# Performance work log

Measured on AMD Instinct MI355X. Metric: run time of the kernel, lower is better.

## Reference

```python
import jax, jax.numpy as jnp
import numpy as np

GRID = 128
N0 = 262144
CHANNELS = [16, 32, 64, 128, 256]
EPS = 1e-5
OFFS2 = [(dx, dy, dz) for dx in (0, 1) for dy in (0, 1) for dz in (0, 1)]
OFFS3 = [(dx, dy, dz) for dx in (-1, 0, 1) for dy in (-1, 0, 1) for dz in (-1, 0, 1)]


def _keys(c, size):
    return (c[:, 0].astype(np.int64) * size + c[:, 1]) * size + c[:, 2]


def _rulebook(in_coords, out_coords, offsets, size_in, stride):
    # explicit-GEMM rulebook: for each kernel offset, (input_idx, output_idx) pairs,
    # padded to n_out with a validity mask so shapes are static.
    ik = _keys(in_coords, size_in)
    order = np.argsort(ik)
    sk = ik[order]
    K, P = len(offsets), out_coords.shape[0]
    I = np.zeros((K, P), np.int32)
    O = np.zeros((K, P), np.int32)
    M = np.zeros((K, P), bool)
    for k, off in enumerate(offsets):
        nbr = out_coords * stride + np.asarray(off)
        valid = np.all((nbr >= 0) & (nbr < size_in), axis=1)
        nk = _keys(np.clip(nbr, 0, size_in - 1), size_in)
        pos = np.minimum(np.searchsorted(sk, nk), len(sk) - 1)
        found = valid & (sk[pos] == nk)
        cnt = int(found.sum())
        I[k, :cnt] = order[pos[found]]
        O[k, :cnt] = np.nonzero(found)[0]
        M[k, :cnt] = True
    return I, O, M


def setup_inputs() -> dict:
    rng = np.random.RandomState(0)
    flat = rng.choice(GRID ** 3, size=N0, replace=False)
    coords = np.stack([flat // (GRID * GRID), (flat // GRID) % GRID, flat % GRID], 1).astype(np.int64)
    key = jax.random.key(0)
    ctr = [0]
    def nrm(shape, scale=1.0):
        ctr[0] += 1
        return scale * jax.random.normal(jax.random.fold_in(key, ctr[0]), shape, jnp.float32)
    inp = {"x": nrm((N0, CHANNELS[0]))}
    size = GRID
    for l in range(4):
        cin, cout = CHANNELS[l], CHANNELS[l + 1]
        out_coords = np.unique(coords // 2, axis=0)
        dI, dO, dM = _rulebook(coords, out_coords, OFFS2, size, 2)       # stride-2, k=2 down conv
        bI, bO, bM = _rulebook(out_coords, out_coords, OFFS3, size // 2, 1)  # stride-1, k=3 block conv
        inp[f"dW{l}"] = nrm((8, cin, cout), (8 * cin) ** -0.5)
        inp[f"dI{l}"] = jnp.asarray(dI); inp[f"dO{l}"] = jnp.asarray(dO); inp[f"dM{l}"] = jnp.asarray(dM)
        inp[f"dG{l}"] = 1.0 + nrm((cout,), 0.1)
        inp[f"dB{l}"] = nrm((cout,), 0.1)
        inp[f"dN{l}"] = int(out_coords.shape[0])
        inp[f"bW{l}"] = nrm((27, cout, cout), (27 * cout) ** -0.5)
        inp[f"bC{l}"] = nrm((cout,), 0.01)
        inp[f"bI{l}"] = jnp.asarray(bI); inp[f"bO{l}"] = jnp.asarray(bO); inp[f"bM{l}"] = jnp.asarray(bM)
        inp[f"bG{l}"] = 1.0 + nrm((cout,), 0.1)
        inp[f"bH{l}"] = nrm((cout,), 0.1)
        coords = out_coords
        size //= 2
    return inp


def _conv(f, W, I, O, M, n_out, bias=None):
    # gather -> GEMM -> scatter-add, one pass per kernel offset (fixed small K)
    out = jnp.zeros((n_out, W.shape[-1]), f.dtype)
    for k in range(W.shape[0]):
        g = jnp.where(M[k][:, None], f[I[k]], 0.0)
        out = out.at[O[k]].add(g @ W[k])
    return out if bias is None else out + bias


def _bn_relu(f, g, b):
    # training-mode BatchNorm over active voxels, fused with ReLU
    m = f.mean(0)
    v = jnp.mean((f - m) ** 2, 0)
    return jax.nn.relu((f - m) * (g * jax.lax.rsqrt(v + EPS)) + b)


def _forward(x, levels):
    outs = [x]
    for (dW, dI, dO, dM, dG, dB, dN, bW, bC, bI, bO, bM, bG, bH) in levels:
        x = _bn_relu(_conv(x, dW, dI, dO, dM, dN), dG, dB)        # down block (bias=False)
        x = _bn_relu(_conv(x, bW, bI, bO, bM, dN, bC), bG, bH)    # ConvBlock
        outs.append(x)
    return tuple(outs)


def reference(x, dW0, dI0, dO0, dM0, dG0, dB0, dN0, bW0, bC0, bI0, bO0, bM0, bG0, bH0,
              dW1, dI1, dO1, dM1, dG1, dB1, dN1, bW1, bC1, bI1, bO1, bM1, bG1, bH1,
              dW2, dI2, dO2, dM2, dG2, dB2, dN2, bW2, bC2, bI2, bO2, bM2, bG2, bH2,
              dW3, dI3, dO3, dM3, dG3, dB3, dN3, bW3, bC3, bI3, bO3, bM3, bG3, bH3):
    levels = [
        (dW0, dI0, dO0, dM0, dG0, dB0, dN0, bW0, bC0, bI0, bO0, bM0, bG0, bH0),
        (dW1, dI1, dO1, dM1, dG1, dB1, dN1, bW1, bC1, bI1, bO1, bM1, bG1, bH1),
        (dW2, dI2, dO2, dM2, dG2, dB2, dN2, bW2, bC2, bI2, bO2, bM2, bG2, bH2),
        (dW3, dI3, dO3, dM3, dG3, dB3, dN3, bW3, bC3, bI3, bO3, bM3, bG3, bH3),
    ]
    return _forward(x, levels)
```

## Files before the change

### kernel.cpp

```cpp
#include <hip/hip_runtime.h>
#include <hip/hip_bf16.h>
#include <stdint.h>
#include <stddef.h>

typedef __hip_bfloat16 bf16;
typedef __attribute__((ext_vector_type(8))) short bf8_t;
typedef __attribute__((ext_vector_type(4))) float f4_t;
static const int CH[5] = {16, 32, 64, 128, 256};

__device__ __forceinline__ float b2f(unsigned short u) {
    return __uint_as_float(((unsigned int)u) << 16);
}
__device__ __forceinline__ unsigned short f2bu(float f) {
    union { bf16 h; unsigned short u; } cv;
    cv.h = __float2bfloat16(f);
    return cv.u;
}
__device__ __forceinline__ void fma4(float4& a, float s, const float4& w) {
    a.x = fmaf(s, w.x, a.x);
    a.y = fmaf(s, w.y, a.y);
    a.z = fmaf(s, w.z, a.z);
    a.w = fmaf(s, w.w, a.w);
}
struct us4 { unsigned short a, b, c, d; };

__global__ void k_sentinel(float* __restrict__ out, float v) {
    if (threadIdx.x == 0) out[0] = v;
}

__global__ void SparseConvEncoder_20633022890309_kernel(
        const unsigned char* __restrict__ bM0, int* __restrict__ flag) {
    if (threadIdx.x == 0) {
        flag[0] = 1;
        flag[1] = 0;
        flag[2] = (bM0[0] == 1 && bM0[1] == 0 && bM0[2] == 0 && bM0[3] == 0 && bM0[4] == 1) ? 1 : 0;
    }
}

__global__ void __launch_bounds__(256) k_copy(const float* __restrict__ x,
                                              float* __restrict__ y, long n) {
    long i = (long)blockIdx.x * 256 + threadIdx.x;
    if (i < n) y[i] = x[i];
}

__global__ void __launch_bounds__(256) k_copytob(const float* __restrict__ x,
                                                 float* __restrict__ y,
                                                 unsigned short* __restrict__ yb, long n) {
    long i = (long)blockIdx.x * 256 + threadIdx.x;
    if (i < n) {
        float v = x[i];
        y[i] = v;
        yb[i] = f2bu(v);
    }
}

__global__ void __launch_bounds__(256) k_wt2(const float* __restrict__ dW,
                                             unsigned short* __restrict__ dWt, int dcin,
                                             const float* __restrict__ bW,
                                             unsigned short* __restrict__ bWt, int bcin,
                                             int cout, long dtot, long btot) {
    long i = (long)blockIdx.x * 256 + threadIdx.x;
    if (i < dtot) {
        long cc = (long)dcin * cout;
        int k = (int)(i / cc);
        int rem = (int)(i % cc);
        int co = rem / dcin, ci = rem % dcin;
        dWt[i] = f2bu(dW[((long)k * dcin + ci) * cout + co]);
    } else if (i < dtot + btot) {
        long j = i - dtot;
        long cc = (long)bcin * cout;
        int k = (int)(j / cc);
        int rem = (int)(j % cc);
        int co = rem / bcin, ci = rem % bcin;
        bWt[j] = f2bu(bW[((long)k * bcin + ci) * cout + co]);
    }
}

__global__ void __launch_bounds__(256) k_scatter(const int* __restrict__ I,
                                                 const int* __restrict__ O,
                                                 const void* __restrict__ M,
                                                 const int* __restrict__ flag,
                                                 int* __restrict__ R, int P, int k0, int cnt) {
    int i = blockIdx.x * 256 + threadIdx.x;
    if (i >= cnt) return;
    long gi = (long)k0 * P + i;
    int m = flag[2] ? ((const int*)M)[gi] : (int)((const unsigned char*)M)[gi];
    if (!m) return;
    R[(long)(i / P) * P + O[gi]] = I[gi];
}

__global__ void __launch_bounds__(256) k_init(float* __restrict__ out,
                                              const float* __restrict__ bias,
                                              long total, int maskC) {
    long i = (long)blockIdx.x * 256 + threadIdx.x;
    if (i < total) out[i] = bias ? bias[i & maskC] : 0.f;
}

template <int CIN, int TN, int MODE, int KT>
__global__ void __launch_bounds__(256, 2) k_mconv(const unsigned short* __restrict__ Xb,
                                                  const unsigned short* __restrict__ Wt,
                                                  const float* __restrict__ bias,
                                                  const int* __restrict__ R,
                                                  float* __restrict__ out,
                                                  int n, int cout, int kcnt, int gs) {
    const int lane = threadIdx.x & 63;
    const int wave = threadIdx.x >> 6;
    const int rt = blockIdx.x * 4 + wave;
    const int row_tiles = (n + 15) >> 4;
    if (rt >= row_tiles) return;
    const int m = lane & 15, q = lane >> 4;
    const int o = rt * 16 + m;
    const int co0 = blockIdx.y * (16 * TN);
    const bf8_t zero = {};

    f4_t acc[TN];
#pragma unroll
    for (int t = 0; t < TN; ++t) {
        if (MODE == 0) {
            float bv = bias ? bias[co0 + t * 16 + m] : 0.f;
            acc[t][0] = bv; acc[t][1] = bv; acc[t][2] = bv; acc[t][3] = bv;
        } else if (MODE == 1) {
#pragma unroll
            for (int g = 0; g < 4; ++g) {
                int row = rt * 16 + q * 4 + g;
                acc[t][g] = (row < n) ? out[(long)row * cout + co0 + t * 16 + m] : 0.f;
            }
        } else {
            acc[t][0] = 0.f; acc[t][1] = 0.f; acc[t][2] = 0.f; acc[t][3] = 0.f;
        }
    }

    bool touched = (MODE != 2);

    if constexpr (KT > 0) {
        int r[KT];
#pragma unroll
        for (int kk = 0; kk < KT; ++kk)
            r[kk] = (o < n) ? R[(long)kk * n + o] : -1;

        if constexpr (CIN == 16) {
            bf8_t a[KT / 2];
#pragma unroll
            for (int p = 0; p < KT / 2; ++p) {
                int rsel = (q < 2) ? r[2 * p] : r[2 * p + 1];
                long ax = (long)((rsel >= 0) ? rsel : 0) * CIN + (q & 1) * 8;
                bf8_t av = *(const bf8_t*)(Xb + ax);
                a[p] = (rsel >= 0) ? av : zero;
            }
            __builtin_amdgcn_sched_barrier(0);
#pragma unroll
            for (int p = 0; p < KT / 2; ++p) {
                int ksel = 2 * p + (q >> 1);
#pragma unroll
                for (int t = 0; t < TN; ++t) {
                    int co = co0 + t * 16 + m;
                    long bx = ((long)ksel * cout + co) * CIN + (q & 1) * 8;
                    bf8_t b = *(const bf8_t*)(Wt + bx);
                    acc[t] = __builtin_amdgcn_mfma_f32_16x16x32_bf16(a[p], b, acc[t], 0, 0, 0);
                }
            }
        } else {
            constexpr int NC = CIN / 32;
            constexpr int GB = (KT * NC * 4 <= 128) ? KT : 9;
            constexpr int NG = (KT + GB - 1) / GB;

#define PRE_GRP(A, G0)                                                              \
    _Pragma("unroll")                                                               \
    for (int j = 0; j < GB; ++j) {                                                  \
        _Pragma("unroll")                                                           \
        for (int cb = 0; cb < NC; ++cb) {                                           \
            int kk = (G0) + j;                                                      \
            long ax = (long)((r[kk] >= 0) ? r[kk] : 0) * CIN + cb * 32 + q * 8;     \
            bf8_t av = *(const bf8_t*)(Xb + ax);                                    \
            A[j][cb] = (r[kk] >= 0) ? av : zero;                                    \
        }                                                                           \
    }

#define CMP_GRP(A, G0)                                                              \
    _Pragma("unroll")                                                               \
    for (int j = 0; j < GB; ++j) {                                                  \
        _Pragma("unroll")                                                           \
        for (int cb = 0; cb < NC; ++cb) {                                           \
            _Pragma("unroll")                                                       \
            for (int t = 0; t < TN; ++t) {                                          \
                int kk = (G0) + j;                                                  \
                int co = co0 + t * 16 + m;                                          \
                long bx = ((long)kk * cout + co) * CIN + cb * 32 + q * 8;           \
                bf8_t b = *(const bf8_t*)(Wt + bx);                                 \
                acc[t] = __builtin_amdgcn_mfma_f32_16x16x32_bf16(A[j][cb], b,       \
                                                                 acc[t], 0, 0, 0);  \
            }                                                                       \
        }                                                                           \
    }

            if constexpr (NG == 1) {
                bf8_t a0[GB][NC];
                PRE_GRP(a0, 0)
                __builtin_amdgcn_sched_barrier(0);
                CMP_GRP(a0, 0)
            } else {
                static_assert(NG == 3, "phase structure assumes 3 groups");
                bf8_t a0[GB][NC];
                bf8_t a1[GB][NC];
                bf8_t a2[GB][NC];
                PRE_GRP(a0, 0)
                PRE_GRP(a1, GB)
                __builtin_amdgcn_sched_barrier(0);
                CMP_GRP(a0, 0)
                __builtin_amdgcn_sched_barrier(0);
                PRE_GRP(a2, 2 * GB)
                __builtin_amdgcn_sched_barrier(0);
                CMP_GRP(a1, GB)
                __builtin_amdgcn_sched_barrier(0);
                CMP_GRP(a2, 2 * GB)
            }
#undef PRE_GRP
#undef CMP_GRP
        }
    } else {
        int ks = 0, ke = kcnt;
        if (MODE == 2) {
            ks = blockIdx.z * gs;
            ke = ks + gs;
            if (ke > kcnt) ke = kcnt;
        }
        constexpr int NC = (CIN >= 32) ? (CIN / 32) : 1;
        constexpr int JB = (CIN >= 128) ? 2 : 4;
        for (int kb = ks; kb < ke; kb += JB) {
            int rj[JB];
#pragma unroll
            for (int j = 0; j < JB; ++j) {
                int kk = kb + j;
                rj[j] = (kk < ke && o < n) ? R[(long)kk * n + o] : -1;
            }
            if (MODE == 2) {
                int any = 0;
#pragma unroll
                for (int j = 0; j < JB; ++j) any |= (rj[j] >= 0) ? 1 : 0;
                if (__ballot(any) == 0ULL) continue;
                touched = true;
            }
            bf8_t a[JB][NC];
#pragma unroll
            for (int j = 0; j < JB; ++j) {
                int kk = kb + j;
                bool inb = (kk < ke) && (rj[j] >= 0);
#pragma unroll
                for (int cb = 0; cb < NC; ++cb) {
                    const bool kval = !(CIN == 16 && q >= 2);
                    const int kbase = (CIN == 16) ? (kval ? q * 8 : 0) : (cb * 32 + q * 8);
                    long ax = (long)(inb ? rj[j] : 0) * CIN + kbase;
                    bf8_t av = *(const bf8_t*)(Xb + ax);
                    a[j][cb] = (inb && kval) ? av : zero;
                }
            }
            __builtin_amdgcn_sched_barrier(0);
#pragma unroll
            for (int j = 0; j < JB; ++j) {
                int kk = kb + j;
                if (kk >= ke) break;
#pragma unroll
                for (int cb = 0; cb < NC; ++cb) {
                    const bool kval = !(CIN == 16 && q >= 2);
                    const int kbase = (CIN == 16) ? (kval ? q * 8 : 0) : (cb * 32 + q * 8);
#pragma unroll
                    for (int t = 0; t < TN; ++t) {
                        int co = co0 + t * 16 + m;
                        long bx = ((long)kk * cout + co) * CIN + kbase;
                        bf8_t bv = *(const bf8_t*)(Wt + bx);
                        bf8_t b = kval ? bv : zero;
                        acc[t] = __builtin_amdgcn_mfma_f32_16x16x32_bf16(a[j][cb], b,
                                                                         acc[t], 0, 0, 0);
                    }
                }
            }
        }
    }

    if (MODE == 2 && !touched) return;
#pragma unroll
    for (int t = 0; t < TN; ++t) {
#pragma unroll
        for (int g = 0; g < 4; ++g) {
            int row = rt * 16 + q * 4 + g;
            if (row >= n) continue;
            float* p = out + (long)row * cout + co0 + t * 16 + m;
            if (MODE == 2) atomicAdd(p, acc[t][g]);
            else *p = acc[t][g];
        }
    }
}

static void mconv_dispatch(int cin, int tn, int mode, int kt, dim3 grd,
                           const unsigned short* Xb, const unsigned short* Wt,
                           const float* bias, const int* R, float* out,
                           int n, int cout, int kcnt, int gs, hipStream_t stream) {
#define MF_(CC, TT, KK)                                                            \
    if (cin == CC && tn == TT && mode == 0 && kt == KK) {                          \
        k_mconv<CC, TT, 0, KK><<<grd, 256, 0, stream>>>(Xb, Wt, bias, R, out, n,   \
                                                        cout, kcnt, gs);           \
        return;                                                                    \
    }
    MF_(16, 2, 8) MF_(32, 2, 8) MF_(32, 4, 8) MF_(64, 2, 8) MF_(64, 4, 8)
    MF_(32, 2, 27) MF_(64, 2, 27) MF_(64, 4, 27)
#undef MF_
#define M3_(CC, TT, MM)                                                            \
    if (cin == CC && tn == TT && mode == MM) {                                     \
        k_mconv<CC, TT, MM, 0><<<grd, 256, 0, stream>>>(Xb, Wt, bias, R, out, n,   \
                                                        cout, kcnt, gs);           \
        return;                                                                    \
    }
#define M2_(CC) M3_(CC, 2, 0) M3_(CC, 2, 1) M3_(CC, 2, 2) \
                M3_(CC, 4, 0) M3_(CC, 4, 1) M3_(CC, 4, 2)
    M2_(16) M2_(32) M2_(64) M2_(128) M2_(256)
#undef M2_
#undef M3_
}

static void run_mconv(const unsigned short* Xb, const unsigned short* Wt,
                      const float* bias, const int* I, const int* O, const void* M,
                      const int* flag, int* R, float* out, int n, int cin, int cout,
                      int K, int G, hipStream_t stream) {
    int rt = (n + 15) / 16;
    int bx = (rt + 3) / 4;
    int tn = (cout >= 64) ? 4 : 2;
    int gy = cout / (16 * tn);
    long bxy = (long)bx * gy;
    int kg = 1;
    if (bxy < 512 && G >= K) {
        kg = (int)((1024 + bxy - 1) / bxy);
        if (kg > K) kg = K;
    }
    int gs = (K + kg - 1) / kg;
    kg = (K + gs - 1) / gs;

    if (kg > 1) {
        int cnt = K * n;
        hipMemsetAsync(R, 0xFF, (size_t)cnt * 4, stream);
        k_scatter<<<(cnt + 255) / 256, 256, 0, stream>>>(I, O, M, flag, R, n, 0, cnt);
        long tot = (long)n * cout;
        k_init<<<(int)((tot + 255) / 256), 256, 0, stream>>>(out, bias, tot, cout - 1);
        mconv_dispatch(cin, tn, 2, 0, dim3(bx, gy, kg), Xb, Wt, bias, R, out,
                       n, cout, K, gs, stream);
    } else {
        for (int k0 = 0; k0 < K; k0 += G) {
            int g = (K - k0 < G) ? (K - k0) : G;
            int cnt = g * n;
            hipMemsetAsync(R, 0xFF, (size_t)cnt * 4, stream);
            k_scatter<<<(cnt + 255) / 256, 256, 0, stream>>>(I, O, M, flag, R, n, k0, cnt);
            int kt = (k0 == 0 && g == K) ? K : 0;
            mconv_dispatch(cin, tn, (k0 == 0) ? 0 : 1, kt, dim3(bx, gy, 1), Xb,
                           Wt + (size_t)k0 * cout * cin, bias, R, out,
                           n, cout, g, g, stream);
        }
    }
}

template <int CIN, int ROWS, int XBF, int MODE>
__global__ void __launch_bounds__(256) k_conv_t(const void* __restrict__ X,
                                                const float* __restrict__ W,
                                                const float* __restrict__ bias,
                                                const int* __restrict__ R,
                                                float* __restrict__ out,
                                                int n, int cout,
                                                int wk0, int kcnt, int gs) {
    const int c4 = threadIdx.x;
    const int by = blockDim.y;
    const int base = blockIdx.x * by * ROWS;
    const float* Xf = (const float*)X;
    const unsigned short* Xb = (const unsigned short*)X;

    int o[ROWS];
    float4 acc[ROWS];
    bool touched[ROWS];
#pragma unroll
    for (int j = 0; j < ROWS; ++j) {
        o[j] = base + j * by + threadIdx.y;
        touched[j] = false;
        acc[j] = make_float4(0.f, 0.f, 0.f, 0.f);
        if (o[j] < n) {
            if (MODE == 0) {
                if (bias) acc[j] = *(const float4*)(bias + c4 * 4);
            } else if (MODE == 1) {
                acc[j] = *(const float4*)(out + (long)o[j] * cout + c4 * 4);
            }
        }
    }
    int ks = 0, ke = kcnt;
    if (MODE == 2) {
        ks = blockIdx.y * gs;
        ke = ks + gs;
        if (ke > kcnt) ke = kcnt;
    }
    for (int kk = ks; kk < ke; ++kk) {
        int r[ROWS];
        bool any = false;
#pragma unroll
        for (int j = 0; j < ROWS; ++j) {
            r[j] = (o[j] < n) ? R[(long)kk * n + o[j]] : -1;
            any = any || (r[j] >= 0);
            touched[j] = touched[j] || (r[j] >= 0);
        }
        if (!any) continue;
        const float* wk = W + ((long)(wk0 + kk) * CIN) * cout + c4 * 4;
#pragma unroll
        for (int ci = 0; ci < CIN; ci += 4) {
            float4 w0 = *(const float4*)(wk + (long)(ci + 0) * cout);
            float4 w1 = *(const float4*)(wk + (long)(ci + 1) * cout);
            float4 w2 = *(const float4*)(wk + (long)(ci + 2) * cout);
            float4 w3 = *(const float4*)(wk + (long)(ci + 3) * cout);
#pragma unroll
            for (int j = 0; j < ROWS; ++j) {
                if (r[j] < 0) continue;
                float x0, x1, x2, x3;
                if (XBF) {
                    us4 u = *(const us4*)(Xb + (long)r[j] * CIN + ci);
                    x0 = b2f(u.a); x1 = b2f(u.b); x2 = b2f(u.c); x3 = b2f(u.d);
                } else {
                    float4 xv = *(const float4*)(Xf + (long)r[j] * CIN + ci);
                    x0 = xv.x; x1 = xv.y; x2 = xv.z; x3 = xv.w;
                }
                fma4(acc[j], x0, w0);
                fma4(acc[j], x1, w1);
                fma4(acc[j], x2, w2);
                fma4(acc[j], x3, w3);
            }
        }
    }
#pragma unroll
    for (int j = 0; j < ROWS; ++j) {
        if (o[j] >= n) continue;
        if (MODE == 2) {
            if (!touched[j]) continue;
            float* p = out + (long)o[j] * cout + c4 * 4;
            atomicAdd(p + 0, acc[j].x);
            atomicAdd(p + 1, acc[j].y);
            atomicAdd(p + 2, acc[j].z);
            atomicAdd(p + 3, acc[j].w);
        } else {
            *(float4*)(out + (long)o[j] * cout + c4 * 4) = acc[j];
        }
    }
}

static void conv_dispatch(int cin, int rows, int xbf, int mode, dim3 grd, dim3 blk,
                          const void* X, const float* W, const float* bias,
                          const int* R, float* out, int n, int cout,
                          int wk0, int kcnt, int gs, hipStream_t stream) {
#define C3_(CC, RR, XB, MM)                                                        \
    if (cin == CC && rows == RR && xbf == XB && mode == MM) {                      \
        k_conv_t<CC, RR, XB, MM><<<grd, blk, 0, stream>>>(X, W, bias, R, out, n,   \
                                                          cout, wk0, kcnt, gs);    \
        return;                                                                    \
    }
#define C2_(CC, RR) C3_(CC, RR, 0, 0) C3_(CC, RR, 0, 1) C3_(CC, RR, 0, 2) \
                    C3_(CC, RR, 1, 0) C3_(CC, RR, 1, 1) C3_(CC, RR, 1, 2)
#define C1_(CC) C2_(CC, 1) C2_(CC, 2) C2_(CC, 4)
    C1_(16) C1_(32) C1_(64) C1_(128) C1_(256)
#undef C1_
#undef C2_
#undef C3_
}

static void run_conv(const void* X, int xbf, const float* W, const float* bias,
                     const int* I, const int* O, const void* M, const int* flag,
                     int* R, float* out, int n, int cin, int cout, int K,
                     int G, hipStream_t stream) {
    int bx = cout / 4, by = 256 / bx;
    int g4 = (n + by * 4 - 1) / (by * 4);
    int g2 = (n + by * 2 - 1) / (by * 2);
    int rows;
    if (g4 >= 1024) rows = 4;
    else if (g2 >= 1024) rows = 2;
    else rows = 1;
    int gridn = (n + by * rows - 1) / (by * rows);
    int kg = 1;
    if (gridn < 768 && G >= K) {
        kg = (2048 + gridn - 1) / gridn;
        if (kg > K) kg = K;
    }
    int gs = (K + kg - 1) / kg;
    kg = (K + gs - 1) / gs;
    dim3 blk(bx, by);
    if (kg > 1) {
        int cnt = K * n;
        hipMemsetAsync(R, 0xFF, (size_t)cnt * 4, stream);
        k_scatter<<<(cnt + 255) / 256, 256, 0, stream>>>(I, O, M, flag, R, n, 0, cnt);
        long tot = (long)n * cout;
        k_init<<<(int)((tot + 255) / 256), 256, 0, stream>>>(out, bias, tot, cout - 1);
        conv_dispatch(cin, rows, xbf, 2, dim3(gridn, kg), blk, X, W, bias, R, out,
                      n, cout, 0, K, gs, stream);
    } else {
        for (int k0 = 0; k0 < K; k0 += G) {
            int g = (K - k0 < G) ? (K - k0) : G;
            int cnt = g * n;
            hipMemsetAsync(R, 0xFF, (size_t)cnt * 4, stream);
            k_scatter<<<(cnt + 255) / 256, 256, 0, stream>>>(I, O, M, flag, R, n, k0, cnt);
            conv_dispatch(cin, rows, xbf, (k0 == 0) ? 0 : 1, dim3(gridn, 1), blk,
                          X, W, bias, R, out, n, cout, k0, g, g, stream);
        }
    }
}

__global__ void __launch_bounds__(256) k_stats(const float* __restrict__ X,
                                               float* __restrict__ sums, int n, int C) {
    int c = threadIdx.x, ty = threadIdx.y, ny = blockDim.y;
    float s1 = 0.f, s2 = 0.f;
    for (int o = blockIdx.x * ny + ty; o < n; o += gridDim.x * ny) {
        float v = X[(long)o * C + c];
        s1 += v;
        s2 += v * v;
    }
    __shared__ float sm[512];
    sm[ty * C + c] = s1;
    sm[256 + ty * C + c] = s2;
    __syncthreads();
    if (ty == 0) {
        for (int t = 1; t < ny; ++t) {
            s1 += sm[t * C + c];
            s2 += sm[256 + t * C + c];
        }
        atomicAdd(&sums[c], s1);
        atomicAdd(&sums[C + c], s2);
    }
}

__global__ void __launch_bounds__(256) k_apply(const float* __restrict__ X,
                                               const float* __restrict__ sums,
                                               const float* __restrict__ g,
                                               const float* __restrict__ b,
                                               void* __restrict__ Y, int ybf,
                                               unsigned short* __restrict__ Y2,
                                               long total, int maskC, int C, float inv_n) {
    long i = (long)blockIdx.x * 256 + threadIdx.x;
    if (i >= total) return;
    int c = (int)(i & (long)maskC);
    float mean = sums[c] * inv_n;
    float var = fmaf(-mean, mean, sums[C + c] * inv_n);
    float sc = g[c] * rsqrtf(var + 1e-5f);
    float sh = fmaf(-mean, sc, b[c]);
    float v = fmaf(X[i], sc, sh);
    v = v > 0.f ? v : 0.f;
    if (ybf) ((unsigned short*)Y)[i] = f2bu(v);
    else     ((float*)Y)[i] = v;
    if (Y2) Y2[i] = f2bu(v);
}

static void run_bn(const float* src, int n, int C, const float* g, const float* b,
                   void* dst, int dst_bf16, unsigned short* dst2,
                   float* sums, hipStream_t stream) {
    hipMemsetAsync(sums, 0, 2 * C * sizeof(float), stream);
    dim3 sblk(C, 256 / C);
    int sgrd = (n + (int)sblk.y - 1) / (int)sblk.y;
    if (sgrd > 1024) sgrd = 1024;
    k_stats<<<sgrd, sblk, 0, stream>>>(src, sums, n, C);
    long tot = (long)n * C;
    k_apply<<<(int)((tot + 255) / 256), 256, 0, stream>>>(src, sums, g, b, dst, dst_bf16,
                                                          dst2, tot, C - 1, C,
                                                          1.0f / (float)n);
}

extern "C" void kernel_launch(void* const* d_in, const int* in_sizes, int n_in,
                              void* d_out, int out_size, void* d_ws, size_t ws_size,
                              hipStream_t stream) {
    float* out = (float*)d_out;

    int stride = 0;
    if (n_in == 57) stride = 14;
    else if (n_in == 53) stride = 13;
    if (!stride) {
        k_sentinel<<<1, 64, 0, stream>>>(out, 10240.f + (float)n_in);
        return;
    }
    static const int o14[13] = {0, 1, 2, 3, 4, 5, 7, 8, 9, 10, 11, 12, 13};
    static const int o13[13] = {0, 1, 2, 3, 4, 5, 6, 7, 8, 9, 10, 11, 12};
    const int* om = (stride == 14) ? o14 : o13;

    long n0 = (long)in_sizes[0];
    int P[4];
    bool ok = (n0 % 16 == 0);
    long total = n0;
    for (int l = 0; l < 4 && ok; ++l) {
        int base = 1 + stride * l;
        int sdI = in_sizes[base + om[1]], sdO = in_sizes[base + om[2]], sdM = in_sizes[base + om[3]];
        int sbI = in_sizes[base + om[8]], sbO = in_sizes[base + om[9]], sbM = in_sizes[base + om[10]];
        if (sdI <= 0 || sdI % 8 != 0 || sdO != sdI || sdM != sdI) { ok = false; break; }
        int p = sdI / 8;
        if (sbI != 27 * p || sbO != sbI || sbM != sbI) { ok = false; break; }
        if (in_sizes[base + om[0]] != 8 * CH[l] * CH[l + 1]) { ok = false; break; }
        if (in_sizes[base + om[6]] != 27 * CH[l + 1] * CH[l + 1]) { ok = false; break; }
        P[l] = p;
        total += (long)p * CH[l + 1];
    }
    if (!ok) {
        k_sentinel<<<1, 64, 0, stream>>>(out, 49152.f);
        return;
    }
    if (total != (long)out_size) {
        k_sentinel<<<1, 64, 0, stream>>>(out, 53248.f);
        return;
    }

    auto al = [](size_t x) { return (x + 255) / 256 * 256; };
    size_t maxBuf = 0, maxP = 0, maxXb = 0;
    long rowsIn[4] = {n0 / 16, P[0], P[1], P[2]};
    for (int l = 0; l < 4; ++l) {
        size_t b = (size_t)P[l] * CH[l + 1];
        if (b > maxBuf) maxBuf = b;
        if ((size_t)P[l] > maxP) maxP = (size_t)P[l];
        size_t xi = (size_t)rowsIn[l] * CH[l];
        if (xi > maxXb) maxXb = xi;
    }
    const size_t fixed = 4096;
    size_t rmin = al(maxP * 4);
    size_t dwt_sz = al((size_t)8 * 128 * 256 * 2);
    size_t bwt_sz = al((size_t)27 * 256 * 256 * 2);
    size_t mf_need = dwt_sz + bwt_sz + al(maxXb * 2) + al(maxBuf * 2) + fixed + rmin;

    if (ws_size >= mf_need) {
        char* wsp = (char*)d_ws;
        unsigned short* dWt = (unsigned short*)wsp; wsp += dwt_sz;
        unsigned short* bWt = (unsigned short*)wsp; wsp += bwt_sz;
        unsigned short* xb = (unsigned short*)wsp;  wsp += al(maxXb * 2);
        unsigned short* bufB = (unsigned short*)wsp; wsp += al(maxBuf * 2);
        float* sums = (float*)wsp; wsp += 1024;
        int* flag = (int*)wsp;     wsp += 2048;
        int* R = (int*)wsp;
        size_t Rbytes = ws_size - (size_t)(wsp - (char*)d_ws);

        SparseConvEncoder_20633022890309_kernel<<<1, 64, 0, stream>>>(
            (const unsigned char*)d_in[1 + om[10]], flag);
        k_copytob<<<(int)((n0 + 255) / 256), 256, 0, stream>>>((const float*)d_in[0],
                                                               out, xb, n0);

        long coff = n0;
        for (int l = 0; l < 4; ++l) {
            int base = 1 + stride * l;
            const float* dW = (const float*)d_in[base + om[0]];
            const int* dI = (const int*)d_in[base + om[1]];
            const int* dO = (const int*)d_in[base + om[2]];
            const void* dM = d_in[base + om[3]];
            const float* dG = (const float*)d_in[base + om[4]];
            const float* dB = (const float*)d_in[base + om[5]];
            const float* bW = (const float*)d_in[base + om[6]];
            const float* bC = (const float*)d_in[base + om[7]];
            const int* bI = (const int*)d_in[base + om[8]];
            const int* bO = (const int*)d_in[base + om[9]];
            const void* bM = d_in[base + om[10]];
            const float* bG = (const float*)d_in[base + om[11]];
            const float* bH = (const float*)d_in[base + om[12]];
            int n = P[l], cin = CH[l], cout = CH[l + 1];

            int G = (int)(Rbytes / ((size_t)n * 4));
            if (G > 27) G = 27;
            if (G < 1) G = 1;

            float* chunkp = out + coff;

            long dwtot = (long)8 * cin * cout;
            long bwtot = (long)27 * cout * cout;
            k_wt2<<<(int)((dwtot + bwtot + 255) / 256), 256, 0, stream>>>(
                dW, dWt, cin, bW, bWt, cout, cout, dwtot, bwtot);

            run_mconv(xb, dWt, nullptr, dI, dO, dM, flag, R, chunkp,
                      n, cin, cout, 8, (G > 8) ? 8 : G, stream);
            run_bn(chunkp, n, cout, dG, dB, bufB, 1, nullptr, sums, stream);

            run_mconv(bufB, bWt, bC, bI, bO, bM, flag, R, chunkp,
                      n, cout, cout, 27, G, stream);
            run_bn(chunkp, n, cout, bG, bH, chunkp, 0,
                   (l < 3) ? xb : nullptr, sums, stream);

            coff += (long)n * cout;
        }
        return;
    }

    int bufB_bf16;
    size_t bufBytes;
    if (ws_size >= fixed + al(maxBuf * 4) + rmin) { bufB_bf16 = 0; bufBytes = al(maxBuf * 4); }
    else if (ws_size >= fixed + al(maxBuf * 2) + rmin) { bufB_bf16 = 1; bufBytes = al(maxBuf * 2); }
    else {
        k_sentinel<<<1, 64, 0, stream>>>(out, 16384.f + (float)(ws_size >> 20));
        return;
    }
    size_t Rbytes = ws_size - fixed - bufBytes;
    char* wsp = (char*)d_ws;
    void* bufB = (void*)wsp;   wsp += bufBytes;
    float* sums = (float*)wsp; wsp += 1024;
    int* flag = (int*)wsp;     wsp += 2048;
    int* R = (int*)wsp;

    SparseConvEncoder_20633022890309_kernel<<<1, 64, 0, stream>>>(
        (const unsigned char*)d_in[1 + om[10]], flag);
    k_copy<<<(int)((n0 + 255) / 256), 256, 0, stream>>>((const float*)d_in[0], out, n0);

    long coff = n0;
    const void* cur_in = d_in[0];
    int cur_xbf = 0;
    for (int l = 0; l < 4; ++l) {
        int base = 1 + stride * l;
        const float* dW = (const float*)d_in[base + om[0]];
        const int* dI = (const int*)d_in[base + om[1]];
        const int* dO = (const int*)d_in[base + om[2]];
        const void* dM = d_in[base + om[3]];
        const float* dG = (const float*)d_in[base + om[4]];
        const float* dB = (const float*)d_in[base + om[5]];
        const float* bW = (const float*)d_in[base + om[6]];
        const float* bC = (const float*)d_in[base + om[7]];
        const int* bI = (const int*)d_in[base + om[8]];
        const int* bO = (const int*)d_in[base + om[9]];
        const void* bM = d_in[base + om[10]];
        const float* bG = (const float*)d_in[base + om[11]];
        const float* bH = (const float*)d_in[base + om[12]];
        int n = P[l], cin = CH[l], cout = CH[l + 1];

        int G = (int)(Rbytes / ((size_t)n * 4));
        if (G > 27) G = 27;
        if (G < 1) G = 1;

        float* chunkp = out + coff;
        run_conv(cur_in, cur_xbf, dW, nullptr, dI, dO, dM, flag, R, chunkp,
                 n, cin, cout, 8, (G > 8) ? 8 : G, stream);
        run_bn(chunkp, n, cout, dG, dB, bufB, bufB_bf16, nullptr, sums, stream);
        run_conv(bufB, bufB_bf16, bW, bC, bI, bO, bM, flag, R, chunkp,
                 n, cout, cout, 27, G, stream);
        run_bn(chunkp, n, cout, bG, bH, chunkp, 0, nullptr, sums, stream);

        cur_in = (const void*)chunkp;
        cur_xbf = 0;
        coff += (long)n * cout;
    }
}
```

Before: 822.1 us.

## Tile weights in MFMA fragment order and use a zero row for missing neighbors

Weights are reordered into per-lane MFMA fragment layout, so each wave's B loads become contiguous 512-byte reads instead of strided ones. The rulebook is padded to a multiple of 16 rows and filled with the index of an appended zero row instead of -1. This removes per-load validity selects and bounds checks in the gather loops. It also removes the early-skip ballot for empty kernel-offset chunks, so fully empty chunks now execute MFMAs, and it slightly loosens the split-K threshold.

```diff
diff --git a/kernel.cpp b/kernel.cpp
--- a/kernel.cpp
+++ b/kernel.cpp
@@ -54,6 +54,21 @@
     }
 }
 
+__device__ __forceinline__ long wt_tiled_src(long j, int cin, int cout) {
+    int e = (int)(j & 7);
+    int l = (int)((j >> 3) & 63);
+    int m = l & 15, q = l >> 4;
+    long u = j >> 9;
+    int NC = cin >> 5;
+    int cout16 = cout >> 4;
+    int cb = (int)(u % NC); u /= NC;
+    int ct = (int)(u % cout16);
+    int kk = (int)(u / cout16);
+    int ci = cb * 32 + q * 8 + e;
+    int co = ct * 16 + m;
+    return ((long)kk * cin + ci) * cout + co;
+}
+
 __global__ void __launch_bounds__(256) k_wt2(const float* __restrict__ dW,
                                              unsigned short* __restrict__ dWt, int dcin,
                                              const float* __restrict__ bW,
@@ -61,32 +76,40 @@
                                              int cout, long dtot, long btot) {
     long i = (long)blockIdx.x * 256 + threadIdx.x;
     if (i < dtot) {
-        long cc = (long)dcin * cout;
-        int k = (int)(i / cc);
-        int rem = (int)(i % cc);
-        int co = rem / dcin, ci = rem % dcin;
-        dWt[i] = f2bu(dW[((long)k * dcin + ci) * cout + co]);
+        if (dcin == 16) {
+            long cc = (long)dcin * cout;
+            int k = (int)(i / cc);
+            int rem = (int)(i % cc);
+            int co = rem / dcin, ci = rem % dcin;
+            dWt[i] = f2bu(dW[((long)k * dcin + ci) * cout + co]);
+        } else {
+            dWt[i] = f2bu(dW[wt_tiled_src(i, dcin, cout)]);
+        }
     } else if (i < dtot + btot) {
         long j = i - dtot;
-        long cc = (long)bcin * cout;
-        int k = (int)(j / cc);
-        int rem = (int)(j % cc);
-        int co = rem / bcin, ci = rem % bcin;
-        bWt[j] = f2bu(bW[((long)k * bcin + ci) * cout + co]);
-    }
+        bWt[j] = f2bu(bW[wt_tiled_src(j, bcin, cout)]);
+    }
+}
+
+__global__ void __launch_bounds__(256) k_prep(int* __restrict__ R, long cnt, int zr,
+                                              unsigned short* __restrict__ zrow, int zc) {
+    long i = (long)blockIdx.x * 256 + threadIdx.x;
+    if (i < cnt) R[i] = zr;
+    if (i < zc) zrow[i] = 0;
 }
 
 __global__ void __launch_bounds__(256) k_scatter(const int* __restrict__ I,
                                                  const int* __restrict__ O,
                                                  const void* __restrict__ M,
                                                  const int* __restrict__ flag,
-                                                 int* __restrict__ R, int P, int k0, int cnt) {
+                                                 int* __restrict__ R, int P, int S,
+                                                 int k0, int cnt) {
     int i = blockIdx.x * 256 + threadIdx.x;
     if (i >= cnt) return;
     long gi = (long)k0 * P + i;
     int m = flag[2] ? ((const int*)M)[gi] : (int)((const unsigned char*)M)[gi];
     if (!m) return;
-    R[(long)(i / P) * P + O[gi]] = I[gi];
+    R[(long)(i / P) * S + O[gi]] = I[gi];
 }
 
 __global__ void __launch_bounds__(256) k_init(float* __restrict__ out,
@@ -108,9 +131,12 @@
     const int rt = blockIdx.x * 4 + wave;
     const int row_tiles = (n + 15) >> 4;
     if (rt >= row_tiles) return;
+    const int n16 = row_tiles << 4;
     const int m = lane & 15, q = lane >> 4;
     const int o = rt * 16 + m;
     const int co0 = blockIdx.y * (16 * TN);
+    const int bt = blockIdx.y * TN;
+    const int cout16 = cout >> 4;
     const bf8_t zero = {};
 
     f4_t acc[TN];
@@ -130,22 +156,18 @@
         }
     }
 
-    bool touched = (MODE != 2);
-
     if constexpr (KT > 0) {
         int r[KT];
 #pragma unroll
         for (int kk = 0; kk < KT; ++kk)
-            r[kk] = (o < n) ? R[(long)kk * n + o] : -1;
+            r[kk] = R[(long)kk * n16 + o];
 
         if constexpr (CIN == 16) {
             bf8_t a[KT / 2];
 #pragma unroll
             for (int p = 0; p < KT / 2; ++p) {
                 int rsel = (q < 2) ? r[2 * p] : r[2 * p + 1];
-                long ax = (long)((rsel >= 0) ? rsel : 0) * CIN + (q & 1) * 8;
-                bf8_t av = *(const bf8_t*)(Xb + ax);
-                a[p] = (rsel >= 0) ? av : zero;
+                a[p] = *(const bf8_t*)(Xb + (long)rsel * CIN + (q & 1) * 8);
             }
             __builtin_amdgcn_sched_barrier(0);
 #pragma unroll
@@ -161,7 +183,7 @@
             }
         } else {
             constexpr int NC = CIN / 32;
-            constexpr int GB = (KT * NC * 4 <= 128) ? KT : 9;
+            constexpr int GB = (KT * NC * 4 <= 128) ? KT : ((KT > 9) ? 9 : KT);
             constexpr int NG = (KT + GB - 1) / GB;
 
 #define PRE_GRP(A, G0)                                                              \
@@ -169,10 +191,7 @@
     for (int j = 0; j < GB; ++j) {                                                  \
         _Pragma("unroll")                                                           \
         for (int cb = 0; cb < NC; ++cb) {                                           \
-            int kk = (G0) + j;                                                      \
-            long ax = (long)((r[kk] >= 0) ? r[kk] : 0) * CIN + cb * 32 + q * 8;     \
-            bf8_t av = *(const bf8_t*)(Xb + ax);                                    \
-            A[j][cb] = (r[kk] >= 0) ? av : zero;                                    \
+            A[j][cb] = *(const bf8_t*)(Xb + (long)r[(G0) + j] * CIN + cb * 32 + q * 8); \
         }                                                                           \
     }
 
@@ -183,9 +202,7 @@
         for (int cb = 0; cb < NC; ++cb) {                                           \
             _Pragma("unroll")                                                       \
             for (int t = 0; t < TN; ++t) {                                          \
-                int kk = (G0) + j;                                                  \
-                int co = co0 + t * 16 + m;                                          \
-                long bx = ((long)kk * cout + co) * CIN + cb * 32 + q * 8;           \
+                long bx = ((((long)((G0) + j) * cout16 + bt + t) * NC + cb) * 64 + lane) * 8; \
                 bf8_t b = *(const bf8_t*)(Wt + bx);                                 \
                 acc[t] = __builtin_amdgcn_mfma_f32_16x16x32_bf16(A[j][cb], b,       \
                                                                  acc[t], 0, 0, 0);  \
@@ -231,27 +248,20 @@
 #pragma unroll
             for (int j = 0; j < JB; ++j) {
                 int kk = kb + j;
-                rj[j] = (kk < ke && o < n) ? R[(long)kk * n + o] : -1;
-            }
-            if (MODE == 2) {
-                int any = 0;
-#pragma unroll
-                for (int j = 0; j < JB; ++j) any |= (rj[j] >= 0) ? 1 : 0;
-                if (__ballot(any) == 0ULL) continue;
-                touched = true;
+                int kc = (kk < ke) ? kk : (ke - 1);
+                rj[j] = R[(long)kc * n16 + o];
             }
             bf8_t a[JB][NC];
 #pragma unroll
             for (int j = 0; j < JB; ++j) {
-                int kk = kb + j;
-                bool inb = (kk < ke) && (rj[j] >= 0);
 #pragma unroll
                 for (int cb = 0; cb < NC; ++cb) {
-                    const bool kval = !(CIN == 16 && q >= 2);
-                    const int kbase = (CIN == 16) ? (kval ? q * 8 : 0) : (cb * 32 + q * 8);
-                    long ax = (long)(inb ? rj[j] : 0) * CIN + kbase;
-                    bf8_t av = *(const bf8_t*)(Xb + ax);
-                    a[j][cb] = (inb && kval) ? av : zero;
+                    if (CIN == 16) {
+                        a[j][cb] = (q < 2) ? *(const bf8_t*)(Xb + (long)rj[j] * CIN + q * 8)
+                                           : zero;
+                    } else {
+                        a[j][cb] = *(const bf8_t*)(Xb + (long)rj[j] * CIN + cb * 32 + q * 8);
+                    }
                 }
             }
             __builtin_amdgcn_sched_barrier(0);
@@ -261,14 +271,17 @@
                 if (kk >= ke) break;
 #pragma unroll
                 for (int cb = 0; cb < NC; ++cb) {
-                    const bool kval = !(CIN == 16 && q >= 2);
-                    const int kbase = (CIN == 16) ? (kval ? q * 8 : 0) : (cb * 32 + q * 8);
 #pragma unroll
                     for (int t = 0; t < TN; ++t) {
-                        int co = co0 + t * 16 + m;
-                        long bx = ((long)kk * cout + co) * CIN + kbase;
-                        bf8_t bv = *(const bf8_t*)(Wt + bx);
-                        bf8_t b = kval ? bv : zero;
+                        bf8_t b;
+                        if (CIN == 16) {
+                            int co = co0 + t * 16 + m;
+                            b = (q < 2) ? *(const bf8_t*)(Wt + ((long)kk * cout + co) * CIN + q * 8)
+                                        : zero;
+                        } else {
+                            long bx = ((((long)kk * cout16 + bt + t) * NC + cb) * 64 + lane) * 8;
+                            b = *(const bf8_t*)(Wt + bx);
+                        }
                         acc[t] = __builtin_amdgcn_mfma_f32_16x16x32_bf16(a[j][cb], b,
                                                                          acc[t], 0, 0, 0);
                     }
@@ -277,7 +290,6 @@
         }
     }
 
-    if (MODE == 2 && !touched) return;
 #pragma unroll
     for (int t = 0; t < TN; ++t) {
 #pragma unroll
@@ -317,27 +329,30 @@
 #undef M3_
 }
 
-static void run_mconv(const unsigned short* Xb, const unsigned short* Wt,
+static void run_mconv(unsigned short* Xb, int nin, const unsigned short* Wt,
                       const float* bias, const int* I, const int* O, const void* M,
                       const int* flag, int* R, float* out, int n, int cin, int cout,
                       int K, int G, hipStream_t stream) {
     int rt = (n + 15) / 16;
+    int n16 = rt * 16;
     int bx = (rt + 3) / 4;
     int tn = (cout >= 64) ? 4 : 2;
     int gy = cout / (16 * tn);
     long bxy = (long)bx * gy;
     int kg = 1;
-    if (bxy < 512 && G >= K) {
+    if (bxy <= 512 && G >= K) {
         kg = (int)((1024 + bxy - 1) / bxy);
         if (kg > K) kg = K;
     }
     int gs = (K + kg - 1) / kg;
     kg = (K + gs - 1) / gs;
+    unsigned short* zrow = Xb + (size_t)nin * cin;
 
     if (kg > 1) {
-        int cnt = K * n;
-        hipMemsetAsync(R, 0xFF, (size_t)cnt * 4, stream);
-        k_scatter<<<(cnt + 255) / 256, 256, 0, stream>>>(I, O, M, flag, R, n, 0, cnt);
+        long cnt = (long)K * n16;
+        k_prep<<<(int)((cnt + 255) / 256), 256, 0, stream>>>(R, cnt, nin, zrow, cin);
+        k_scatter<<<(K * n + 255) / 256, 256, 0, stream>>>(I, O, M, flag, R, n, n16,
+                                                           0, K * n);
         long tot = (long)n * cout;
         k_init<<<(int)((tot + 255) / 256), 256, 0, stream>>>(out, bias, tot, cout - 1);
         mconv_dispatch(cin, tn, 2, 0, dim3(bx, gy, kg), Xb, Wt, bias, R, out,
@@ -345,9 +360,10 @@
     } else {
         for (int k0 = 0; k0 < K; k0 += G) {
             int g = (K - k0 < G) ? (K - k0) : G;
-            int cnt = g * n;
-            hipMemsetAsync(R, 0xFF, (size_t)cnt * 4, stream);
-            k_scatter<<<(cnt + 255) / 256, 256, 0, stream>>>(I, O, M, flag, R, n, k0, cnt);
+            long cnt = (long)g * n16;
+            k_prep<<<(int)((cnt + 255) / 256), 256, 0, stream>>>(R, cnt, nin, zrow, cin);
+            k_scatter<<<(g * n + 255) / 256, 256, 0, stream>>>(I, O, M, flag, R, n, n16,
+                                                               k0, g * n);
             int kt = (k0 == 0 && g == K) ? K : 0;
             mconv_dispatch(cin, tn, (k0 == 0) ? 0 : 1, kt, dim3(bx, gy, 1), Xb,
                            Wt + (size_t)k0 * cout * cin, bias, R, out,
@@ -485,7 +501,7 @@
     if (kg > 1) {
         int cnt = K * n;
         hipMemsetAsync(R, 0xFF, (size_t)cnt * 4, stream);
-        k_scatter<<<(cnt + 255) / 256, 256, 0, stream>>>(I, O, M, flag, R, n, 0, cnt);
+        k_scatter<<<(cnt + 255) / 256, 256, 0, stream>>>(I, O, M, flag, R, n, n, 0, cnt);
         long tot = (long)n * cout;
         k_init<<<(int)((tot + 255) / 256), 256, 0, stream>>>(out, bias, tot, cout - 1);
         conv_dispatch(cin, rows, xbf, 2, dim3(gridn, kg), blk, X, W, bias, R, out,
@@ -495,7 +511,7 @@
             int g = (K - k0 < G) ? (K - k0) : G;
             int cnt = g * n;
             hipMemsetAsync(R, 0xFF, (size_t)cnt * 4, stream);
-            k_scatter<<<(cnt + 255) / 256, 256, 0, stream>>>(I, O, M, flag, R, n, k0, cnt);
+            k_scatter<<<(cnt + 255) / 256, 256, 0, stream>>>(I, O, M, flag, R, n, n, k0, cnt);
             conv_dispatch(cin, rows, xbf, (k0 == 0) ? 0 : 1, dim3(gridn, 1), blk,
                           X, W, bias, R, out, n, cout, k0, g, g, stream);
         }
@@ -612,17 +628,19 @@
         if (xi > maxXb) maxXb = xi;
     }
     const size_t fixed = 4096;
-    size_t rmin = al(maxP * 4);
+    size_t rmin = al((maxP + 16) * 4);
     size_t dwt_sz = al((size_t)8 * 128 * 256 * 2);
     size_t bwt_sz = al((size_t)27 * 256 * 256 * 2);
-    size_t mf_need = dwt_sz + bwt_sz + al(maxXb * 2) + al(maxBuf * 2) + fixed + rmin;
+    size_t xb_sz = al(maxXb * 2 + 1024);
+    size_t bufB_sz = al(maxBuf * 2 + 1024);
+    size_t mf_need = dwt_sz + bwt_sz + xb_sz + bufB_sz + fixed + rmin;
 
     if (ws_size >= mf_need) {
         char* wsp = (char*)d_ws;
         unsigned short* dWt = (unsigned short*)wsp; wsp += dwt_sz;
         unsigned short* bWt = (unsigned short*)wsp; wsp += bwt_sz;
-        unsigned short* xb = (unsigned short*)wsp;  wsp += al(maxXb * 2);
-        unsigned short* bufB = (unsigned short*)wsp; wsp += al(maxBuf * 2);
+        unsigned short* xb = (unsigned short*)wsp;  wsp += xb_sz;
+        unsigned short* bufB = (unsigned short*)wsp; wsp += bufB_sz;
         float* sums = (float*)wsp; wsp += 1024;
         int* flag = (int*)wsp;     wsp += 2048;
         int* R = (int*)wsp;
@@ -650,8 +668,10 @@
             const float* bG = (const float*)d_in[base + om[11]];
             const float* bH = (const float*)d_in[base + om[12]];
             int n = P[l], cin = CH[l], cout = CH[l + 1];
-
-            int G = (int)(Rbytes / ((size_t)n * 4));
+            int nin = (int)rowsIn[l];
+            int n16 = (n + 15) / 16 * 16;
+
+            int G = (int)(Rbytes / ((size_t)n16 * 4));
             if (G > 27) G = 27;
             if (G < 1) G = 1;
 
@@ -662,11 +682,11 @@
             k_wt2<<<(int)((dwtot + bwtot + 255) / 256), 256, 0, stream>>>(
                 dW, dWt, cin, bW, bWt, cout, cout, dwtot, bwtot);
 
-            run_mconv(xb, dWt, nullptr, dI, dO, dM, flag, R, chunkp,
+            run_mconv(xb, nin, dWt, nullptr, dI, dO, dM, flag, R, chunkp,
                       n, cin, cout, 8, (G > 8) ? 8 : G, stream);
             run_bn(chunkp, n, cout, dG, dB, bufB, 1, nullptr, sums, stream);
 
-            run_mconv(bufB, bWt, bC, bI, bO, bM, flag, R, chunkp,
+            run_mconv(bufB, n, bWt, bC, bI, bO, bM, flag, R, chunkp,
                       n, cout, cout, 27, G, stream);
             run_bn(chunkp, n, cout, bG, bH, chunkp, 0,
                    (l < 3) ? xb : nullptr, sums, stream);
```

Result: faster. 783.2 us (-4.7%).
